# Kernel tuning notes

Hardware: AMD Instinct MI355X
Metric: run time of the kernel (lower is better)

The kernel has to match this reference:

```python
import jax, jax.numpy as jnp
import numpy as np

N_NODES = 50000

def setup_inputs() -> dict:
    key = jax.random.key(0)
    ks = jax.random.split(key, 8)
    d_in, d_h = 128, 128
    x = jax.random.normal(ks[0], (N_NODES, d_in), dtype=jnp.float32)
    edge_index = jax.random.randint(ks[1], (2, 800000), 0, N_NODES, dtype=jnp.int64)
    edge_pairs = jax.random.randint(ks[2], (1000000, 2), 0, N_NODES, dtype=jnp.int64)
    W_gcn = jax.random.normal(ks[3], (d_in, d_h), dtype=jnp.float32) / np.sqrt(d_in)
    b_gcn = jnp.zeros((d_h,), dtype=jnp.float32)
    W1 = jax.random.normal(ks[4], (2 * d_h, d_h), dtype=jnp.float32) / np.sqrt(2 * d_h)
    b1 = jnp.zeros((d_h,), dtype=jnp.float32)
    W2 = jax.random.normal(ks[5], (d_h, 1), dtype=jnp.float32) / np.sqrt(d_h)
    b2 = jnp.zeros((1,), dtype=jnp.float32)
    return {"x": x, "edge_index": edge_index, "edge_pairs": edge_pairs,
            "W_gcn": W_gcn, "b_gcn": b_gcn, "W1": W1, "b1": b1, "W2": W2, "b2": b2}

def gcn_conv(x, edge_index, W, b):
    # PyG GCNConv default: add self-loops, symmetric normalization.
    n = x.shape[0]
    loop = jnp.arange(n, dtype=edge_index.dtype)
    src = jnp.concatenate([edge_index[0], loop])  # [E+N]
    dst = jnp.concatenate([edge_index[1], loop])
    deg = jax.ops.segment_sum(jnp.ones(src.shape[0], dtype=x.dtype), dst, num_segments=n)
    dinv = jnp.where(deg > 0, jax.lax.rsqrt(deg), 0.0)
    norm = dinv[src] * dinv[dst]                  # [E+N]
    h = x @ W                                     # [N, H]
    agg = jax.ops.segment_sum(h[src] * norm[:, None], dst, num_segments=n)
    return agg + b

def reference(x, edge_index, edge_pairs, W_gcn, b_gcn, W1, b1, W2, b2):
    h = gcn_conv(x, edge_index, W_gcn, b_gcn)      # [N, H]
    e = jnp.concatenate([h[edge_pairs[:, 0]], h[edge_pairs[:, 1]]], axis=-1)  # [P, 2H]
    edge_logits = jax.nn.relu(e @ W1 + b1) @ W2 + b2  # [P, 1]
    return edge_logits, edge_pairs, h
```

## Files before the change

kernel.cpp:

```cpp
#include <hip/hip_runtime.h>
#include <hip/hip_fp16.h>

#define WG 256

typedef _Float16 f16;
typedef _Float16 hv2 __attribute__((ext_vector_type(2)));
typedef _Float16 f16x4 __attribute__((ext_vector_type(4)));
typedef _Float16 f16x8 __attribute__((ext_vector_type(8)));
typedef float f32x4 __attribute__((ext_vector_type(4)));

__global__ __launch_bounds__(WG) void k_misc0(const float* __restrict__ Wg,
                                              f16* __restrict__ Wgt,
                                              const float* __restrict__ W1,
                                              f16* __restrict__ W1t) {
    int b = blockIdx.x;
    if (b < 64) {
        int i = b * WG + threadIdx.x;
        int k = i & 127, nI = i >> 7;
        Wgt[i] = (f16)Wg[(size_t)k * 128 + nI];
    } else {
        int i = (b - 64) * WG + threadIdx.x;
        int k = i & 255, nI = i >> 8;
        W1t[i] = (f16)W1[(size_t)k * 128 + nI];
    }
}

__global__ __launch_bounds__(WG) void k_fusedA(const float* __restrict__ A,
                                               const f16* __restrict__ Wt,
                                               __half2* __restrict__ Out, int n,
                                               const int* __restrict__ dst,
                                               int* __restrict__ deg,
                                               int* __restrict__ rank, int e,
                                               const int* __restrict__ pairs,
                                               float* __restrict__ outp, int n4,
                                               int* __restrict__ pcount,
                                               int* __restrict__ pboff, int slice,
                                               int nmm, int necnt, int ncvt) {
    __shared__ __align__(16) char smem[64 * 136 * 2];
    int b = blockIdx.x, slot = b & 3, idx = b >> 2;
    int tid = threadIdx.x;
    if (slot == 1 || slot == 3) {
        int hid = idx * 2 + (slot >> 1);
        if (hid >= necnt) return;
        int i = hid * WG + tid;
        if (i < e) rank[i] = atomicAdd(&deg[dst[i]], 1);
        return;
    }
    if (slot == 2) {
        if (idx >= ncvt) return;
        int* hist = (int*)smem;
        if (tid < 8) hist[tid] = 0;
        __syncthreads();
        int i = idx * WG + tid;
        if (i < n4) {
            int4 v = ((const int4*)pairs)[i];
            ((float4*)outp)[i] = make_float4((float)v.x, (float)v.y, (float)v.z, (float)v.w);
            atomicAdd(&hist[v.x / slice], 1);
            atomicAdd(&hist[v.z / slice], 1);
        }
        __syncthreads();
        if (tid < 8) pboff[idx * 8 + tid] = atomicAdd(&pcount[tid], hist[tid]);
        return;
    }
    if (idx >= nmm) return;
    f16(*Bs)[136] = (f16(*)[136])smem;
    const int row0 = idx * 64;
    const int wv = tid >> 6, lane = tid & 63, m = lane & 15, quad = lane >> 4;
    const int arow = row0 + wv * 16 + m;
    f16x8 af[4];
    if (arow < n) {
#pragma unroll
        for (int kk = 0; kk < 4; ++kk) {
            const float* ap = A + (size_t)arow * 128 + kk * 32 + quad * 8;
            float4 v0 = *(const float4*)ap;
            float4 v1 = *(const float4*)(ap + 4);
            af[kk] = (f16x8){(f16)v0.x, (f16)v0.y, (f16)v0.z, (f16)v0.w,
                             (f16)v1.x, (f16)v1.y, (f16)v1.z, (f16)v1.w};
        }
    } else {
#pragma unroll
        for (int kk = 0; kk < 4; ++kk)
            af[kk] = (f16x8){(f16)0.f, (f16)0.f, (f16)0.f, (f16)0.f,
                             (f16)0.f, (f16)0.f, (f16)0.f, (f16)0.f};
    }
    f32x4 acc[8];
#pragma unroll
    for (int t = 0; t < 8; ++t) acc[t] = (f32x4){0.f, 0.f, 0.f, 0.f};
#pragma unroll
    for (int half = 0; half < 2; ++half) {
        for (int f = tid; f < 64 * 16; f += WG) {
            int r = f >> 4, c = f & 15;
            *(float4*)&Bs[r][c * 8] = ((const float4*)Wt)[(half * 64 + r) * 16 + c];
        }
        __syncthreads();
#pragma unroll
        for (int kk = 0; kk < 4; ++kk) {
#pragma unroll
            for (int t = 0; t < 4; ++t) {
                f16x8 bf = *(f16x8*)&Bs[t * 16 + m][kk * 32 + quad * 8];
                acc[half * 4 + t] =
                    __builtin_amdgcn_mfma_f32_16x16x32_f16(af[kk], bf, acc[half * 4 + t], 0, 0, 0);
            }
        }
        __syncthreads();
    }
#pragma unroll
    for (int r = 0; r < 4; ++r) {
        int row = row0 + wv * 16 + quad * 4 + r;
        if (row < n) {
#pragma unroll
            for (int t = 0; t < 4; ++t)
                Out[(size_t)row * 64 + t * 16 + m] =
                    __floats2half2_rn(acc[t][r], acc[t + 4][r]);
        }
    }
}

__global__ __launch_bounds__(WG) void k_scan1(const int* __restrict__ deg,
                                              float* __restrict__ dinv,
                                              int* __restrict__ base,
                                              int* __restrict__ bsum, int n) {
    __shared__ int t[WG];
    int tid = threadIdx.x;
    int i = blockIdx.x * WG + tid;
    int v = (i < n) ? deg[i] : 0;
    if (i < n) dinv[i] = rsqrtf((float)(v + 1));
    t[tid] = v;
    __syncthreads();
    for (int o = 1; o < WG; o <<= 1) {
        int add = (tid >= o) ? t[tid - o] : 0;
        __syncthreads();
        t[tid] += add;
        __syncthreads();
    }
    if (i < n) base[i] = t[tid] - v;
    if (tid == WG - 1) bsum[blockIdx.x] = t[WG - 1];
}

__global__ __launch_bounds__(WG) void k_scan23(int* __restrict__ base,
                                               const int* __restrict__ bsum,
                                               int n, int e, int nb) {
    __shared__ int t[WG];
    int tid = threadIdx.x;
    int v = (tid < nb) ? bsum[tid] : 0;
    t[tid] = v;
    __syncthreads();
    for (int o = 1; o < WG; o <<= 1) {
        int add = (tid >= o) ? t[tid - o] : 0;
        __syncthreads();
        t[tid] += add;
        __syncthreads();
    }
    int off = t[blockIdx.x] - ((blockIdx.x < nb) ? bsum[blockIdx.x] : 0);
    int i = blockIdx.x * WG + tid;
    if (i < n) {
        base[i] += off;
        if (i == n - 1) base[n] = e;
    }
}

__global__ __launch_bounds__(WG) void k_fill(const int* __restrict__ src,
                                             const int* __restrict__ dst,
                                             const int* __restrict__ base,
                                             const int* __restrict__ rank,
                                             int* __restrict__ esrc, int e) {
    int i = blockIdx.x * WG + threadIdx.x;
    if (i >= e) return;
    esrc[base[dst[i]] + rank[i]] = src[i];
}

__global__ __launch_bounds__(WG) void k_gather(const __half2* __restrict__ Hpk,
                                               const float* __restrict__ dinv,
                                               const float* __restrict__ bg,
                                               const int* __restrict__ base,
                                               const int* __restrict__ esrc,
                                               float* __restrict__ outh, int n) {
    int tid = threadIdx.x;
    int node = blockIdx.x * 16 + (tid >> 4);
    int sub = tid & 15;
    if (node >= n) return;
    float dv = dinv[node];
    int4 hh = *(const int4*)(Hpk + (size_t)node * 64 + 4 * sub);
    const int* hp = (const int*)&hh;
    float accl[4], acch[4];
#pragma unroll
    for (int k = 0; k < 4; ++k) {
        hv2 h = __builtin_bit_cast(hv2, hp[k]);
        accl[k] = (float)h[0] * dv;
        acch[k] = (float)h[1] * dv;
    }
    const int j = base[node], jend = base[node + 1];
    for (int j0 = j; j0 < jend; j0 += 8) {
        int s[8];
#pragma unroll
        for (int t = 0; t < 8; ++t) {
            int jt = j0 + t;
            s[t] = esrc[jt < jend ? jt : jend - 1];
        }
        float ds[8];
#pragma unroll
        for (int t = 0; t < 8; ++t) ds[t] = (j0 + t < jend) ? dinv[s[t]] : 0.f;
        int4 r[8];
#pragma unroll
        for (int t = 0; t < 8; ++t)
            r[t] = *(const int4*)(Hpk + (size_t)s[t] * 64 + 4 * sub);
#pragma unroll
        for (int t = 0; t < 8; ++t) {
            const int* pr = (const int*)&r[t];
#pragma unroll
            for (int k = 0; k < 4; ++k) {
                hv2 h = __builtin_bit_cast(hv2, pr[k]);
                accl[k] = fmaf((float)h[0], ds[t], accl[k]);
                acch[k] = fmaf((float)h[1], ds[t], acch[k]);
            }
        }
    }
    float4 blo = *(const float4*)(bg + 4 * sub);
    float4 bhi = *(const float4*)(bg + 4 * sub + 64);
    *(float4*)&outh[(size_t)node * 128 + 4 * sub] =
        make_float4(fmaf(accl[0], dv, blo.x), fmaf(accl[1], dv, blo.y),
                    fmaf(accl[2], dv, blo.z), fmaf(accl[3], dv, blo.w));
    *(float4*)&outh[(size_t)node * 128 + 64 + 4 * sub] =
        make_float4(fmaf(acch[0], dv, bhi.x), fmaf(acch[1], dv, bhi.y),
                    fmaf(acch[2], dv, bhi.z), fmaf(acch[3], dv, bhi.w));
}

__global__ __launch_bounds__(WG) void k_fusedE(const float* __restrict__ A,
                                               const f16* __restrict__ W1t,
                                               const float* __restrict__ b1,
                                               __half2* __restrict__ Up,
                                               __half2* __restrict__ Vp, int n, int nmm,
                                               const int* __restrict__ pairs,
                                               const int* __restrict__ pcount,
                                               const int* __restrict__ pboff,
                                               int2* __restrict__ plist2,
                                               int n4, int ncvt, int slice) {
    __shared__ __align__(16) char smem[64 * 136 * 2];
    int b = blockIdx.x, slot = b & 1, idx = b >> 1;
    const int tid = threadIdx.x;
    if (slot == 1) {
        if (idx >= ncvt) return;
        int* cnt8 = (int*)smem;
        if (tid < 8) cnt8[tid] = 0;
        __syncthreads();
        int i = idx * WG + tid;
        if (i < n4) {
            int gb[8];
            int run = 0;
#pragma unroll
            for (int k = 0; k < 8; ++k) { gb[k] = run; run += pcount[k]; }
            int4 v = ((const int4*)pairs)[i];
            int bk0 = v.x / slice;
            int r0 = atomicAdd(&cnt8[bk0], 1);
            plist2[gb[bk0] + pboff[idx * 8 + bk0] + r0] =
                make_int2(v.y | ((v.x - bk0 * slice) << 16), 2 * i);
            int bk1 = v.z / slice;
            int r1 = atomicAdd(&cnt8[bk1], 1);
            plist2[gb[bk1] + pboff[idx * 8 + bk1] + r1] =
                make_int2(v.w | ((v.z - bk1 * slice) << 16), 2 * i + 1);
        }
        return;
    }
    if (idx >= nmm) return;
    f16(*Bs)[136] = (f16(*)[136])smem;
    const int row0 = idx * 64;
    const int wv = tid >> 6, lane = tid & 63, m = lane & 15, quad = lane >> 4;
    const int arow = row0 + wv * 16 + m;
    f16x8 af[4];
    if (arow < n) {
#pragma unroll
        for (int kk = 0; kk < 4; ++kk) {
            const float* ap = A + (size_t)arow * 128 + kk * 32 + quad * 8;
            float4 v0 = *(const float4*)ap;
            float4 v1 = *(const float4*)(ap + 4);
            af[kk] = (f16x8){(f16)v0.x, (f16)v0.y, (f16)v0.z, (f16)v0.w,
                             (f16)v1.x, (f16)v1.y, (f16)v1.z, (f16)v1.w};
        }
    } else {
#pragma unroll
        for (int kk = 0; kk < 4; ++kk)
            af[kk] = (f16x8){(f16)0.f, (f16)0.f, (f16)0.f, (f16)0.f,
                             (f16)0.f, (f16)0.f, (f16)0.f, (f16)0.f};
    }
    f32x4 acc[8];
#pragma unroll
    for (int ph = 0; ph < 2; ++ph) {
#pragma unroll
        for (int t = 0; t < 8; ++t) acc[t] = (f32x4){0.f, 0.f, 0.f, 0.f};
#pragma unroll
        for (int half = 0; half < 2; ++half) {
            for (int f = tid; f < 64 * 16; f += WG) {
                int r = f >> 4, c = f & 15;
                *(float4*)&Bs[r][c * 8] =
                    *(const float4*)(W1t + (size_t)(half * 64 + r) * 256 + ph * 128 + c * 8);
            }
            __syncthreads();
#pragma unroll
            for (int kk = 0; kk < 4; ++kk) {
#pragma unroll
                for (int t = 0; t < 4; ++t) {
                    f16x8 bf = *(f16x8*)&Bs[t * 16 + m][kk * 32 + quad * 8];
                    acc[half * 4 + t] =
                        __builtin_amdgcn_mfma_f32_16x16x32_f16(af[kk], bf, acc[half * 4 + t], 0, 0, 0);
                }
            }
            __syncthreads();
        }
        __half2* Out = ph ? Vp : Up;
#pragma unroll
        for (int t = 0; t < 4; ++t) {
            float bl = 0.f, bh = 0.f;
            if (!ph) { bl = b1[t * 16 + m]; bh = b1[t * 16 + m + 64]; }
#pragma unroll
            for (int r = 0; r < 4; ++r) {
                int row = row0 + wv * 16 + quad * 4 + r;
                if (row < n)
                    Out[(size_t)row * 64 + t * 16 + m] =
                        __floats2half2_rn(acc[t][r] + bl, acc[t + 4][r] + bh);
            }
        }
    }
}

__global__ __launch_bounds__(WG) void k_pairx(const __half2* __restrict__ U,
                                              const __half2* __restrict__ V,
                                              const float* __restrict__ W2,
                                              const float* __restrict__ b2,
                                              const int* __restrict__ pcount,
                                              const int2* __restrict__ plist2,
                                              float* __restrict__ out_logit,
                                              int slice) {
    const int bkt = blockIdx.x & 7, blkid = blockIdx.x >> 3, NB = gridDim.x >> 3;
    int gbase = 0, cnt;
    {
        int c[8];
#pragma unroll
        for (int k = 0; k < 8; ++k) c[k] = pcount[k];
#pragma unroll
        for (int k = 0; k < 8; ++k)
            if (k < bkt) gbase += c[k];
        cnt = c[bkt];
    }
    const int2* pl = plist2 + gbase;
    const int abase = bkt * slice;
    const int lane = threadIdx.x & 63, wv = threadIdx.x >> 6;
    const int g = lane >> 4, sub = lane & 15;

    float4 w2lo = ((const float4*)W2)[sub];
    float4 w2hi = ((const float4*)(W2 + 64))[sub];
    hv2 w2h[4];
    w2h[0] = hv2{(f16)w2lo.x, (f16)w2hi.x};
    w2h[1] = hv2{(f16)w2lo.y, (f16)w2hi.y};
    w2h[2] = hv2{(f16)w2lo.z, (f16)w2hi.z};
    w2h[3] = hv2{(f16)w2lo.w, (f16)w2hi.w};
    const float bb = b2[0];
    const hv2 z2 = hv2{(f16)0.f, (f16)0.f};

    for (int pos = blkid * 128 + wv * 32; pos < cnt; pos += NB * 128) {
        int q0 = pos + g;
        if (q0 >= cnt) continue;
        int q[8];
        q[0] = q0;
#pragma unroll
        for (int t = 1; t < 8; ++t) {
            int qt = q0 + 4 * t;
            q[t] = (qt < cnt) ? qt : q0;
        }
        int2 e[8];
#pragma unroll
        for (int t = 0; t < 8; ++t) e[t] = pl[q[t]];
        int4 uu[8], vv[8];
#pragma unroll
        for (int t = 0; t < 8; ++t) {
            int a = abase + (e[t].x >> 16);
            int bi = e[t].x & 0xFFFF;
            uu[t] = *(const int4*)(U + (size_t)a * 64 + 4 * sub);
            vv[t] = *(const int4*)(V + (size_t)bi * 64 + 4 * sub);
        }
        float p[8];
#pragma unroll
        for (int t = 0; t < 8; ++t) p[t] = 0.f;
#pragma unroll
        for (int k = 0; k < 4; ++k) {
#pragma unroll
            for (int t = 0; t < 8; ++t) {
                const int* ui = (const int*)&uu[t];
                const int* vi = (const int*)&vv[t];
                hv2 s = __builtin_bit_cast(hv2, ui[k]) + __builtin_bit_cast(hv2, vi[k]);
                p[t] = __builtin_amdgcn_fdot2(__builtin_elementwise_max(s, z2), w2h[k],
                                              p[t], false);
            }
        }
#pragma unroll
        for (int m = 1; m < 16; m <<= 1) {
#pragma unroll
            for (int t = 0; t < 8; ++t) p[t] += __shfl_xor(p[t], m, 64);
        }
        if (sub == 0) {
            out_logit[e[0].y] = p[0] + bb;
#pragma unroll
            for (int t = 1; t < 8; ++t)
                if (q0 + 4 * t < cnt) out_logit[e[t].y] = p[t] + bb;
        }
    }
}

extern "C" void kernel_launch(void* const* d_in, const int* in_sizes, int n_in,
                              void* d_out, int out_size, void* d_ws, size_t ws_size,
                              hipStream_t stream) {
    const float* x     = (const float*)d_in[0];
    const int*   eidx  = (const int*)d_in[1];
    const int*   pairs = (const int*)d_in[2];
    const float* W_gcn = (const float*)d_in[3];
    const float* b_gcn = (const float*)d_in[4];
    const float* W1    = (const float*)d_in[5];
    const float* b1    = (const float*)d_in[6];
    const float* W2    = (const float*)d_in[7];
    const float* b2    = (const float*)d_in[8];

    const int N = in_sizes[0] / 128;
    const int E = in_sizes[1] / 2;
    const int P = in_sizes[2] / 2;
    const int* esrc_in = eidx;
    const int* edst_in = eidx + E;
    const int slice = (N + 7) / 8;

    float* ws      = (float*)d_ws;
    int*   deg     = (int*)d_ws;
    int*   pcount  = (int*)d_ws + N;
    float* dinv    = ws + 65536;
    int*   base    = (int*)(ws + 131072);
    int*   bsum    = (int*)(ws + 196608);
    f16*   Wt_gcn  = (f16*)(ws + 197120);
    f16*   W1t     = (f16*)(ws + 205312);
    int*   pboff   = (int*)(ws + 221696);
    int*   rank    = (int*)(ws + 238080);
    int*   ecsr    = rank + (size_t)E;
    __half2* Hpk   = (__half2*)(ecsr + (size_t)E);
    __half2* Upk   = Hpk + (size_t)N * 64;
    __half2* Vpk   = Upk + (size_t)N * 64;
    int2*  plist2  = (int2*)Hpk;

    float* out_logit = (float*)d_out;
    float* out_pairs = out_logit + P;
    float* out_h     = out_logit + 3 * (size_t)P;

    const int nb    = (N + WG - 1) / WG;
    const int nmm   = (N + 63) / 64;
    const int necnt = (E + WG - 1) / WG;
    const int ncvt  = (P / 2 + WG - 1) / WG;
    int gmax = nmm;
    int h2 = (necnt + 1) / 2;
    if (h2 > gmax) gmax = h2;
    if (ncvt > gmax) gmax = ncvt;
    int emax = (nmm > ncvt) ? nmm : ncvt;
    dim3 blk(WG);

    hipMemsetAsync(deg, 0, (size_t)N * 4 + 32, stream);
    k_misc0  <<<192, blk, 0, stream>>>(W_gcn, Wt_gcn, W1, W1t);
    k_fusedA <<<4 * gmax, blk, 0, stream>>>(x, Wt_gcn, Hpk, N,
                                            edst_in, deg, rank, E,
                                            pairs, out_pairs, P / 2,
                                            pcount, pboff, slice,
                                            nmm, necnt, ncvt);
    k_scan1  <<<nb, blk, 0, stream>>>(deg, dinv, base, bsum, N);
    k_scan23 <<<nb, blk, 0, stream>>>(base, bsum, N, E, nb);
    k_fill   <<<necnt, blk, 0, stream>>>(esrc_in, edst_in, base, rank, ecsr, E);
    k_gather <<<(N + 15) / 16, blk, 0, stream>>>(Hpk, dinv, b_gcn, base, ecsr, out_h, N);
    k_fusedE <<<2 * emax, blk, 0, stream>>>(out_h, W1t, b1, Upk, Vpk, N, nmm,
                                            pairs, pcount, pboff, plist2,
                                            P / 2, ncvt, slice);
    k_pairx  <<<4096, blk, 0, stream>>>(Upk, Vpk, W2, b2, pcount, plist2,
                                        out_logit, slice);
}
```

Baseline: 261.0 us.

## Pack dinv with CSR sources and move pair conversion into the gather kernel

The fill kernel now writes (src, dinv[src]) pairs into the CSR array, so the gather loop no longer performs a dependent random load of dinv per edge. The pair-to-float conversion and slice histogram work moves out of the first fused kernel and is interleaved with the gather kernel's blocks. The first kernel's grid becomes a two-way interleave of matmul and degree-count blocks. The cost is a CSR array twice as large, which means more fill writes and more gather read bandwidth.

Measured after the change: 267.3 us. 1.02x slower.

```diff
diff --git a/kernel.cpp b/kernel.cpp
--- a/kernel.cpp
+++ b/kernel.cpp
@@ -31,35 +31,14 @@
                                                const int* __restrict__ dst,
                                                int* __restrict__ deg,
                                                int* __restrict__ rank, int e,
-                                               const int* __restrict__ pairs,
-                                               float* __restrict__ outp, int n4,
-                                               int* __restrict__ pcount,
-                                               int* __restrict__ pboff, int slice,
-                                               int nmm, int necnt, int ncvt) {
+                                               int nmm, int necnt) {
     __shared__ __align__(16) char smem[64 * 136 * 2];
-    int b = blockIdx.x, slot = b & 3, idx = b >> 2;
+    int b = blockIdx.x, slot = b & 1, idx = b >> 1;
     int tid = threadIdx.x;
-    if (slot == 1 || slot == 3) {
-        int hid = idx * 2 + (slot >> 1);
-        if (hid >= necnt) return;
-        int i = hid * WG + tid;
+    if (slot == 1) {
+        if (idx >= necnt) return;
+        int i = idx * WG + tid;
         if (i < e) rank[i] = atomicAdd(&deg[dst[i]], 1);
-        return;
-    }
-    if (slot == 2) {
-        if (idx >= ncvt) return;
-        int* hist = (int*)smem;
-        if (tid < 8) hist[tid] = 0;
-        __syncthreads();
-        int i = idx * WG + tid;
-        if (i < n4) {
-            int4 v = ((const int4*)pairs)[i];
-            ((float4*)outp)[i] = make_float4((float)v.x, (float)v.y, (float)v.z, (float)v.w);
-            atomicAdd(&hist[v.x / slice], 1);
-            atomicAdd(&hist[v.z / slice], 1);
-        }
-        __syncthreads();
-        if (tid < 8) pboff[idx * 8 + tid] = atomicAdd(&pcount[tid], hist[tid]);
         return;
     }
     if (idx >= nmm) return;
@@ -163,20 +142,45 @@
                                              const int* __restrict__ dst,
                                              const int* __restrict__ base,
                                              const int* __restrict__ rank,
-                                             int* __restrict__ esrc, int e) {
+                                             const float* __restrict__ dinv,
+                                             int2* __restrict__ ecsr2, int e) {
     int i = blockIdx.x * WG + threadIdx.x;
     if (i >= e) return;
-    esrc[base[dst[i]] + rank[i]] = src[i];
+    int s = src[i];
+    ecsr2[base[dst[i]] + rank[i]] = make_int2(s, __float_as_int(dinv[s]));
 }
 
 __global__ __launch_bounds__(WG) void k_gather(const __half2* __restrict__ Hpk,
                                                const float* __restrict__ dinv,
                                                const float* __restrict__ bg,
                                                const int* __restrict__ base,
-                                               const int* __restrict__ esrc,
-                                               float* __restrict__ outh, int n) {
+                                               const int2* __restrict__ ecsr2,
+                                               float* __restrict__ outh, int n, int ngath,
+                                               const int* __restrict__ pairs,
+                                               float* __restrict__ outp, int n4,
+                                               int* __restrict__ pcount,
+                                               int* __restrict__ pboff, int slice,
+                                               int ncvt) {
+    __shared__ int hist[8];
+    int b = blockIdx.x, role = b & 1, idx = b >> 1;
     int tid = threadIdx.x;
-    int node = blockIdx.x * 16 + (tid >> 4);
+    if (role == 1) {
+        if (idx >= ncvt) return;
+        if (tid < 8) hist[tid] = 0;
+        __syncthreads();
+        int i = idx * WG + tid;
+        if (i < n4) {
+            int4 v = ((const int4*)pairs)[i];
+            ((float4*)outp)[i] = make_float4((float)v.x, (float)v.y, (float)v.z, (float)v.w);
+            atomicAdd(&hist[v.x / slice], 1);
+            atomicAdd(&hist[v.z / slice], 1);
+        }
+        __syncthreads();
+        if (tid < 8) pboff[idx * 8 + tid] = atomicAdd(&pcount[tid], hist[tid]);
+        return;
+    }
+    if (idx >= ngath) return;
+    int node = idx * 16 + (tid >> 4);
     int sub = tid & 15;
     if (node >= n) return;
     float dv = dinv[node];
@@ -191,19 +195,20 @@
     }
     const int j = base[node], jend = base[node + 1];
     for (int j0 = j; j0 < jend; j0 += 8) {
-        int s[8];
+        int2 ee[8];
 #pragma unroll
         for (int t = 0; t < 8; ++t) {
             int jt = j0 + t;
-            s[t] = esrc[jt < jend ? jt : jend - 1];
+            ee[t] = ecsr2[jt < jend ? jt : jend - 1];
         }
         float ds[8];
 #pragma unroll
-        for (int t = 0; t < 8; ++t) ds[t] = (j0 + t < jend) ? dinv[s[t]] : 0.f;
+        for (int t = 0; t < 8; ++t)
+            ds[t] = (j0 + t < jend) ? __int_as_float(ee[t].y) : 0.f;
         int4 r[8];
 #pragma unroll
         for (int t = 0; t < 8; ++t)
-            r[t] = *(const int4*)(Hpk + (size_t)s[t] * 64 + 4 * sub);
+            r[t] = *(const int4*)(Hpk + (size_t)ee[t].x * 64 + 4 * sub);
 #pragma unroll
         for (int t = 0; t < 8; ++t) {
             const int* pr = (const int*)&r[t];
@@ -435,8 +440,8 @@
     f16*   W1t     = (f16*)(ws + 205312);
     int*   pboff   = (int*)(ws + 221696);
     int*   rank    = (int*)(ws + 238080);
-    int*   ecsr    = rank + (size_t)E;
-    __half2* Hpk   = (__half2*)(ecsr + (size_t)E);
+    int2*  ecsr2   = (int2*)(rank + (size_t)E);
+    __half2* Hpk   = (__half2*)(ecsr2 + (size_t)E);
     __half2* Upk   = Hpk + (size_t)N * 64;
     __half2* Vpk   = Upk + (size_t)N * 64;
     int2*  plist2  = (int2*)Hpk;
@@ -449,24 +454,23 @@
     const int nmm   = (N + 63) / 64;
     const int necnt = (E + WG - 1) / WG;
     const int ncvt  = (P / 2 + WG - 1) / WG;
-    int gmax = nmm;
-    int h2 = (necnt + 1) / 2;
-    if (h2 > gmax) gmax = h2;
-    if (ncvt > gmax) gmax = ncvt;
-    int emax = (nmm > ncvt) ? nmm : ncvt;
+    const int ngath = (N + 15) / 16;
+    int gmaxA = (nmm > necnt) ? nmm : necnt;
+    int gmaxG = (ngath > ncvt) ? ngath : ncvt;
+    int emax  = (nmm > ncvt) ? nmm : ncvt;
     dim3 blk(WG);
 
     hipMemsetAsync(deg, 0, (size_t)N * 4 + 32, stream);
     k_misc0  <<<192, blk, 0, stream>>>(W_gcn, Wt_gcn, W1, W1t);
-    k_fusedA <<<4 * gmax, blk, 0, stream>>>(x, Wt_gcn, Hpk, N,
-                                            edst_in, deg, rank, E,
-                                            pairs, out_pairs, P / 2,
-                                            pcount, pboff, slice,
-                                            nmm, necnt, ncvt);
+    k_fusedA <<<2 * gmaxA, blk, 0, stream>>>(x, Wt_gcn, Hpk, N,
+                                             edst_in, deg, rank, E, nmm, necnt);
     k_scan1  <<<nb, blk, 0, stream>>>(deg, dinv, base, bsum, N);
     k_scan23 <<<nb, blk, 0, stream>>>(base, bsum, N, E, nb);
-    k_fill   <<<necnt, blk, 0, stream>>>(esrc_in, edst_in, base, rank, ecsr, E);
-    k_gather <<<(N + 15) / 16, blk, 0, stream>>>(Hpk, dinv, b_gcn, base, ecsr, out_h, N);
+    k_fill   <<<necnt, blk, 0, stream>>>(esrc_in, edst_in, base, rank, dinv, ecsr2, E);
+    k_gather <<<2 * gmaxG, blk, 0, stream>>>(Hpk, dinv, b_gcn, base, ecsr2,
+                                             out_h, N, ngath,
+                                             pairs, out_pairs, P / 2,
+                                             pcount, pboff, slice, ncvt);
     k_fusedE <<<2 * emax, blk, 0, stream>>>(out_h, W1t, b1, Upk, Vpk, N, nmm,
                                             pairs, pcount, pboff, plist2,
                                             P / 2, ncvt, slice);
```
